# Kernel tuning notes

Hardware: AMD Instinct MI355X
Metric: run time of the kernel (lower is better)

## Reference

```python
import jax, jax.numpy as jnp
import numpy as np

EPS = 1e-7
NUM_ROUTING = 3


def squash(s, axis=-1):
    # v = ||s||^2/(1+||s||^2) * s/||s||, numerically safe
    sq = jnp.sum(jnp.square(s), axis=axis, keepdims=True)
    scale = sq / (1.0 + sq) / jnp.sqrt(sq + EPS)
    return scale * s


def setup_inputs() -> dict:
    key = jax.random.key(0)
    k1, k2 = jax.random.split(key)
    B, IN_CAPS, IN_DIM = 256, 1152, 8
    NUM_CAPS, DIM_VEC = 10, 16
    inputs = jax.random.normal(k1, (B, IN_CAPS, IN_DIM), dtype=jnp.float32)
    # glorot_uniform over [in_caps, num_caps, dim_vec, in_dim]
    limit = np.sqrt(6.0 / (IN_DIM + DIM_VEC))
    W = jax.random.uniform(k2, (IN_CAPS, NUM_CAPS, DIM_VEC, IN_DIM), dtype=jnp.float32,
                           minval=-limit, maxval=limit)
    bias = jnp.zeros((IN_CAPS, NUM_CAPS), dtype=jnp.float32)
    return {"inputs": inputs, "W": W, "bias": bias}


def reference(inputs, W, bias):
    # u_hat[b,i,c,d] = W[i,c,d,e] @ inputs[b,i,e]
    u_hat = jnp.einsum('icde,bie->bicd', W, inputs)  # [B, in_caps, num_caps, dim_vec]
    b = bias[None]  # [1, in_caps, num_caps], broadcasts to [B, ...]
    for _ in range(NUM_ROUTING - 1):
        c = jax.nn.softmax(b, axis=2)                       # over num_capsule
        s = jnp.einsum('bic,bicd->bcd', c * jnp.ones_like(u_hat[..., 0]), u_hat)
        v = squash(s, axis=-1)                              # [B, num_caps, dim_vec]
        agreement = jnp.einsum('bicd,bcd->bic', u_hat, v)
        b = agreement + b + bias[None]
    c_last = jax.nn.softmax(b, axis=2)
    s = jnp.einsum('bic,bicd->bcd', c_last * jnp.ones_like(u_hat[..., 0]), u_hat)
    outputs = squash(s, axis=-1)                            # [B, num_caps, dim_vec]
    return outputs
```

## Files before the change

### kernel.cpp

```cpp
#include <hip/hip_runtime.h>
#include <math.h>

#define BATCH 256
#define IC    1152
#define EDIM  8
#define NC    10
#define DV    16

#define ITILE  8
#define NCHUNK 6
#define ITOT   (ITILE * NCHUNK)
#define NB     4
#define NTHREADS 256
#define NWAVES 4
#define NSLAB  (IC / ITOT)
#define BCHUNKS (BATCH / NB)
#define SCD (NC * DV)
#define SPART_STRIDE (BATCH * SCD)
#define L2E 1.4426950408889634f
#define XF4_TOT (NB * ITOT * EDIM / 4)
#define XF4_ROW (ITOT * EDIM / 4)
#define WXU     2560
#define WT_F4   (NSLAB * NCHUNK * WXU)

typedef float v2f __attribute__((ext_vector_type(2)));
typedef float v4f __attribute__((ext_vector_type(4)));

template<int CTRL>
__device__ __forceinline__ float dpp_add(float x) {
    int r = __builtin_amdgcn_update_dpp(0, __float_as_int(x), CTRL, 0xF, 0xF, true);
    return x + __int_as_float(r);
}
__device__ __forceinline__ float row_reduce16(float x) {
    x = dpp_add<0xB1>(x);
    x = dpp_add<0x4E>(x);
    x = dpp_add<0x141>(x);
    x = dpp_add<0x140>(x);
    return x;
}

typedef int int2v __attribute__((ext_vector_type(2)));
#if __has_builtin(__builtin_amdgcn_permlane32_swap)
__device__ __forceinline__ float cross32_sum(float x) {
    int2v r = __builtin_amdgcn_permlane32_swap(__float_as_int(x), __float_as_int(x),
                                               false, false);
    return __int_as_float(r[0]) + __int_as_float(r[1]);
}
#else
__device__ __forceinline__ float cross32_sum(float x) { return x + __shfl_xor(x, 32); }
#endif

#if __has_builtin(__builtin_amdgcn_exp2f)
#define EXP2F(x) __builtin_amdgcn_exp2f(x)
#else
#define EXP2F(x) exp2f(x)
#endif

__device__ __forceinline__ float dot8_pk(v4f w0, v4f w1, v4f x0, v4f x1) {
    v2f a =  __builtin_shufflevector(w0, w0, 0, 1) * __builtin_shufflevector(x0, x0, 0, 1);
    a = __builtin_elementwise_fma(__builtin_shufflevector(w0, w0, 2, 3),
                                  __builtin_shufflevector(x0, x0, 2, 3), a);
    a = __builtin_elementwise_fma(__builtin_shufflevector(w1, w1, 0, 1),
                                  __builtin_shufflevector(x1, x1, 0, 1), a);
    a = __builtin_elementwise_fma(__builtin_shufflevector(w1, w1, 2, 3),
                                  __builtin_shufflevector(x1, x1, 2, 3), a);
    return a[0] + a[1];
}

__global__ __launch_bounds__(256)
void caps_wxform(const float4* __restrict__ W4, float4* __restrict__ Wt)
{
    __shared__ float4 lds[WXU];
    const int tid = threadIdx.x;
    const size_t base = (size_t)blockIdx.x * WXU;

    #pragma unroll
    for (int t = 0; t < WXU / 256; ++t)
        lds[t * 256 + tid] = W4[base + t * 256 + tid];
    __syncthreads();
    #pragma unroll
    for (int t = 0; t < WXU / 256; ++t) {
        int lo   = t * 256 + tid;
        int wid  = lo / 640;
        int r0   = lo - wid * 640;
        int kk   = r0 >> 7;
        int r1   = r0 & 127;
        int h    = r1 >> 6;
        int ch   = (r1 >> 5) & 1;
        int il_lo= (r1 >> 4) & 1;
        int d    = r1 & 15;
        int il   = wid * 2 + il_lo;
        int c    = ch * 5 + kk;
        Wt[base + lo] = lds[il * 320 + c * 32 + d * 2 + h];
    }
}

template<int MODE>
__global__ __launch_bounds__(NTHREADS, 2)
void caps_main(const float* __restrict__ x,
               const v4f* __restrict__ Wt,
               const float* __restrict__ bias,
               const float* __restrict__ v_in,
               float* __restrict__ b2,
               float* __restrict__ s_part)
{
    __shared__ float sx[NB][ITOT * EDIM];
    __shared__ float swv[NWAVES][NB][SCD];
    __shared__ float vls[NB][SCD];

    const int tid = threadIdx.x;
    const int d   = tid & 15;
    const int ch  = (tid >> 5) & 1;
    const int il  = ((tid >> 4) & 1) | (((tid >> 6) & 3) << 1);
    const int wid = tid >> 6;
    const int icb = blockIdx.x;
    const int bcb = blockIdx.y;
    const int i0  = icb * ITOT;
    const int b0  = bcb * NB;

    {
        const float4* xg = (const float4*)x;
        float4* xs = (float4*)&sx[0][0];
        #pragma unroll
        for (int t = 0; t < 2; ++t) {
            int idx = t * NTHREADS + tid;
            if (idx < XF4_TOT) {
                int bb = idx / XF4_ROW;
                int w  = idx - bb * XF4_ROW;
                xs[idx] = xg[(size_t)(b0 + bb) * (IC * EDIM / 4)
                             + i0 * (EDIM / 4) + w];
            }
        }
    }
    if (MODE != 1) {
        #pragma unroll
        for (int t = 0; t < 3; ++t) {
            int j = t * NTHREADS + tid;
            if (j < NB * SCD)
                (&vls[0][0])[j] = v_in[(size_t)b0 * SCD + j];
        }
    }

    float sacc[NB][5];
    #pragma unroll
    for (int bb = 0; bb < NB; ++bb)
        #pragma unroll
        for (int k = 0; k < 5; ++k) sacc[bb][k] = 0.f;

    __syncthreads();

    const v4f* wpb = Wt + (size_t)((icb * NCHUNK) * NWAVES + wid) * 640
                        + (tid & 63);

    #pragma unroll 1
    for (int ic = 0; ic < NCHUNK; ++ic) {
        const int i = i0 + ic * ITILE + il;
        const v4f* wp = wpb + (size_t)ic * (NWAVES * 640);

        v4f   w4[5][2];
        float bv[5];
        #pragma unroll
        for (int k = 0; k < 5; ++k) {
            w4[k][0] = wp[(k * 2 + 0) * 64];
            w4[k][1] = wp[(k * 2 + 1) * 64];
            bv[k]    = bias[i * NC + ch * 5 + k];
        }

        float cw[5];
        float bvs[5];
        if (MODE == 1) {
            float ssum = 0.f, ex[5];
            #pragma unroll
            for (int k = 0; k < 5; ++k) { ex[k] = __expf(bv[k]); ssum += ex[k]; }
            ssum = cross32_sum(ssum);
            float inv = __builtin_amdgcn_rcpf(ssum);
            #pragma unroll
            for (int k = 0; k < 5; ++k) cw[k] = ex[k] * inv;
        } else {
            #pragma unroll
            for (int k = 0; k < 5; ++k) bvs[k] = bv[k] * L2E;
        }

        #pragma unroll
        for (int bb = 0; bb < NB; ++bb) {
            const int b = b0 + bb;
            const v4f x0 = ((const v4f*)&sx[bb][(ic * ITILE + il) * EDIM])[0];
            const v4f x1 = ((const v4f*)&sx[bb][(ic * ITILE + il) * EDIM])[1];

            float u[5];
            #pragma unroll
            for (int k = 0; k < 5; ++k)
                u[k] = dot8_pk(w4[k][0], w4[k][1], x0, x1);

            if (MODE != 1) {
                const float* vb = &vls[bb][ch * 80 + d];
                float t[5];
                #pragma unroll
                for (int k = 0; k < 5; ++k) t[k] = u[k] * vb[k * 16];
                #pragma unroll
                for (int k = 0; k < 5; ++k) t[k] = row_reduce16(t[k]);

                float br[5];
                float* bp = b2 + (((size_t)b * IC + i) * 2 + ch) * 8;
                if (MODE == 2) {
                    #pragma unroll
                    for (int k = 0; k < 5; ++k) br[k] = fmaf(2.0f, bvs[k], t[k]);
                    if (d == 0) {
                        #pragma unroll
                        for (int k = 0; k < 5; ++k) bp[k] = br[k];
                    }
                } else {
                    #pragma unroll
                    for (int k = 0; k < 5; ++k) br[k] = t[k] + bp[k] + bvs[k];
                }
                float ssum = 0.f, ex[5];
                #pragma unroll
                for (int k = 0; k < 5; ++k) { ex[k] = EXP2F(br[k]); ssum += ex[k]; }
                ssum = cross32_sum(ssum);
                float inv = __builtin_amdgcn_rcpf(ssum);
                #pragma unroll
                for (int k = 0; k < 5; ++k) cw[k] = ex[k] * inv;
            }

            #pragma unroll
            for (int k = 0; k < 5; ++k)
                sacc[bb][k] = fmaf(cw[k], u[k], sacc[bb][k]);
        }
    }

    #pragma unroll
    for (int bb = 0; bb < NB; ++bb) {
        #pragma unroll
        for (int k = 0; k < 5; ++k) {
            float s = sacc[bb][k] + __shfl_xor(sacc[bb][k], 16);
            if ((tid & 16) == 0)
                swv[wid][bb][ch * 80 + k * 16 + d] = s;
        }
    }
    __syncthreads();
    for (int j = tid; j < NB * SCD; j += NTHREADS) {
        int bb = j / SCD;
        int cd = j - bb * SCD;
        float s = (swv[0][bb][cd] + swv[1][bb][cd])
                + (swv[2][bb][cd] + swv[3][bb][cd]);
        s_part[((size_t)icb * BATCH + b0 + bb) * SCD + cd] = s;
    }
}

__global__ __launch_bounds__(256)
void caps_squash(const float* __restrict__ s_part, float* __restrict__ out,
                 float mult)
{
    const int tid = threadIdx.x;
    const int bc  = blockIdx.x * 16 + (tid >> 4);
    const size_t off = (size_t)bc * DV + (tid & 15);

    float a[4] = {0.f, 0.f, 0.f, 0.f};
    #pragma unroll
    for (int ic = 0; ic < NSLAB; ic += 4) {
        #pragma unroll
        for (int j = 0; j < 4; ++j)
            a[j] += s_part[(size_t)(ic + j) * SPART_STRIDE + off];
    }
    float s = (a[0] + a[1]) + (a[2] + a[3]);

    float sq = row_reduce16(s * s);

    float scale = sq / ((1.0f + sq) * sqrtf(sq + 1e-7f));
    out[off] = (mult * scale) * s;
}

extern "C" void kernel_launch(void* const* d_in, const int* in_sizes, int n_in,
                              void* d_out, int out_size, void* d_ws, size_t ws_size,
                              hipStream_t stream)
{
    const float* x    = (const float*)d_in[0];
    const float* W    = (const float*)d_in[1];
    const float* bias = (const float*)d_in[2];
    float* out = (float*)d_out;

    float* ws     = (float*)d_ws;
    float* s_part = ws;
    float* v      = s_part + (size_t)NSLAB * SPART_STRIDE;
    float* b2     = v + SPART_STRIDE;
    float* wt     = b2 + (size_t)BATCH * IC * 16;

    dim3 grid(NSLAB, BCHUNKS);

    caps_wxform<<<NSLAB * NCHUNK, 256, 0, stream>>>((const float4*)W, (float4*)wt);

    caps_main<1><<<grid, NTHREADS, 0, stream>>>(x, (const v4f*)wt, bias, v, b2, s_part);
    caps_squash<<<160, 256, 0, stream>>>(s_part, v, L2E);
    caps_main<2><<<grid, NTHREADS, 0, stream>>>(x, (const v4f*)wt, bias, v, b2, s_part);
    caps_squash<<<160, 256, 0, stream>>>(s_part, v, L2E);
    caps_main<3><<<grid, NTHREADS, 0, stream>>>(x, (const v4f*)wt, bias, v, b2, s_part);
    caps_squash<<<160, 256, 0, stream>>>(s_part, out, 1.0f);
}
```

Baseline: 163.4 us.

## Fuse partial-sum reduction and squash into next routing kernel prologue

Removes the two intermediate squash launches by having each caps_main block reduce the per-slab partial sums for its batch rows and apply squash itself. The partial-sum buffers are ping-ponged between two workspace regions so that reads and writes of consecutive iterations do not alias. This eliminates launch gaps and a global round trip for v, at the cost of every slab block redundantly reading all slab partials for its batch chunk.

```diff
diff --git a/kernel.cpp b/kernel.cpp
--- a/kernel.cpp
+++ b/kernel.cpp
@@ -17,6 +17,7 @@
 #define BCHUNKS (BATCH / NB)
 #define SCD (NC * DV)
 #define SPART_STRIDE (BATCH * SCD)
+#define SPART_F4     (SPART_STRIDE / 4)
 #define L2E 1.4426950408889634f
 #define XF4_TOT (NB * ITOT * EDIM / 4)
 #define XF4_ROW (ITOT * EDIM / 4)
@@ -36,6 +37,11 @@
     x = dpp_add<0x4E>(x);
     x = dpp_add<0x141>(x);
     x = dpp_add<0x140>(x);
+    return x;
+}
+__device__ __forceinline__ float quad_reduce4(float x) {
+    x = dpp_add<0xB1>(x);
+    x = dpp_add<0x4E>(x);
     return x;
 }
 
@@ -100,7 +106,7 @@
 void caps_main(const float* __restrict__ x,
                const v4f* __restrict__ Wt,
                const float* __restrict__ bias,
-               const float* __restrict__ v_in,
+               const float* __restrict__ s_in,
                float* __restrict__ b2,
                float* __restrict__ s_part)
 {
@@ -133,11 +139,21 @@
         }
     }
     if (MODE != 1) {
-        #pragma unroll
-        for (int t = 0; t < 3; ++t) {
-            int j = t * NTHREADS + tid;
-            if (j < NB * SCD)
-                (&vls[0][0])[j] = v_in[(size_t)b0 * SCD + j];
+        if (tid < NB * SCD / 4) {
+            const v4f* sp = (const v4f*)s_in + (size_t)b0 * (SCD / 4) + tid;
+            v4f a0 = {0.f,0.f,0.f,0.f}, a1 = a0, a2 = a0, a3 = a0;
+            #pragma unroll
+            for (int ic = 0; ic < NSLAB; ic += 4) {
+                a0 += sp[(ic + 0) * SPART_F4];
+                a1 += sp[(ic + 1) * SPART_F4];
+                a2 += sp[(ic + 2) * SPART_F4];
+                a3 += sp[(ic + 3) * SPART_F4];
+            }
+            v4f s4 = (a0 + a1) + (a2 + a3);
+            float sq = (s4[0]*s4[0] + s4[1]*s4[1]) + (s4[2]*s4[2] + s4[3]*s4[3]);
+            sq = quad_reduce4(sq);
+            float scale = L2E * sq / ((1.0f + sq) * sqrtf(sq + 1e-7f));
+            ((v4f*)&vls[0][0])[tid] = scale * s4;
         }
     }
 
@@ -248,8 +264,7 @@
 }
 
 __global__ __launch_bounds__(256)
-void caps_squash(const float* __restrict__ s_part, float* __restrict__ out,
-                 float mult)
+void caps_squash(const float* __restrict__ s_part, float* __restrict__ out)
 {
     const int tid = threadIdx.x;
     const int bc  = blockIdx.x * 16 + (tid >> 4);
@@ -267,7 +282,7 @@
     float sq = row_reduce16(s * s);
 
     float scale = sq / ((1.0f + sq) * sqrtf(sq + 1e-7f));
-    out[off] = (mult * scale) * s;
+    out[off] = scale * s;
 }
 
 extern "C" void kernel_launch(void* const* d_in, const int* in_sizes, int n_in,
@@ -280,19 +295,17 @@
     float* out = (float*)d_out;
 
     float* ws     = (float*)d_ws;
-    float* s_part = ws;
-    float* v      = s_part + (size_t)NSLAB * SPART_STRIDE;
-    float* b2     = v + SPART_STRIDE;
+    float* sA     = ws;
+    float* sB     = sA + (size_t)NSLAB * SPART_STRIDE;
+    float* b2     = sB + (size_t)NSLAB * SPART_STRIDE;
     float* wt     = b2 + (size_t)BATCH * IC * 16;
 
     dim3 grid(NSLAB, BCHUNKS);
 
     caps_wxform<<<NSLAB * NCHUNK, 256, 0, stream>>>((const float4*)W, (float4*)wt);
 
-    caps_main<1><<<grid, NTHREADS, 0, stream>>>(x, (const v4f*)wt, bias, v, b2, s_part);
-    caps_squash<<<160, 256, 0, stream>>>(s_part, v, L2E);
-    caps_main<2><<<grid, NTHREADS, 0, stream>>>(x, (const v4f*)wt, bias, v, b2, s_part);
-    caps_squash<<<160, 256, 0, stream>>>(s_part, v, L2E);
-    caps_main<3><<<grid, NTHREADS, 0, stream>>>(x, (const v4f*)wt, bias, v, b2, s_part);
-    caps_squash<<<160, 256, 0, stream>>>(s_part, out, 1.0f);
-}
+    caps_main<1><<<grid, NTHREADS, 0, stream>>>(x, (const v4f*)wt, bias, nullptr, b2, sA);
+    caps_main<2><<<grid, NTHREADS, 0, stream>>>(x, (const v4f*)wt, bias, sA, b2, sB);
+    caps_main<3><<<grid, NTHREADS, 0, stream>>>(x, (const v4f*)wt, bias, sB, b2, sA);
+    caps_squash<<<160, 256, 0, stream>>>(sA, out);
+}
```

After: 169.8 us. +4.0%, slower.
